# Optimization experiments

Measured on AMD Instinct MI355X. Metric: run time of the kernel, lower is better.

## Reference

```python
import jax, jax.numpy as jnp
import numpy as np

B, S, T, D, H, FF = 4, 96, 96, 512, 8, 2048
DK = D // H
EPS = 1e-5
NEG_SLOPE = 0.01  # LeakyReLU default


def setup_inputs() -> dict:
    key = jax.random.key(0)
    ks = jax.random.split(key, 8)
    w = lambda k, shape: jax.random.normal(k, shape, jnp.float32) * 0.02
    return {
        "x": jax.random.normal(ks[0], (B, S, T, D), jnp.float32),
        "mask_bias": jax.random.uniform(ks[1], (B, S, T), jnp.float32),
        "t_w": w(ks[2], (4, D, D)), "t_b": jnp.zeros((4, D), jnp.float32),
        "s_w": w(ks[3], (4, D, D)), "s_b": jnp.zeros((4, D), jnp.float32),
        "fc_w1": w(ks[4], (D, FF)), "fc_b1": jnp.zeros((FF,), jnp.float32),
        "fc_w2": w(ks[5], (FF, D)), "fc_b2": jnp.zeros((D,), jnp.float32),
        "ln1_g": jnp.ones((D,), jnp.float32), "ln1_b": jnp.zeros((D,), jnp.float32),
        "ln2_g": jnp.ones((D,), jnp.float32), "ln2_b": jnp.zeros((D,), jnp.float32),
    }


def _ln(y, g, b):
    m = y.mean(-1, keepdims=True)
    v = ((y - m) ** 2).mean(-1, keepdims=True)
    return (y - m) / jnp.sqrt(v + EPS) * g + b


def _split_heads(y):
    # (B,S,T,D) -> (B,H,S,T,DK)
    b, s, t, _ = y.shape
    return y.reshape(b, s, t, H, DK).transpose(0, 3, 1, 2, 4)


def _mha(x, w, b, mask_bias, time_axis):
    q = _split_heads(x @ w[0] + b[0])
    k = _split_heads(x @ w[1] + b[1])
    v = _split_heads(x @ w[2] + b[2])
    scale = 1.0 / np.sqrt(DK)
    if time_axis:
        # attention over time axis T: scores (B,H,S,T,T)
        p = jax.nn.softmax(jnp.einsum('bhstd,bhsud->bhstu', q, k) * scale, axis=-1)
        p = p * mask_bias[:, None, :, :, None]            # post-softmax mask
        o = jnp.einsum('bhstu,bhsud->bhstd', p, v)
    else:
        # attention over space axis S: scores (B,H,T,S,S)
        p = jax.nn.softmax(jnp.einsum('bhstd,bhutd->bhtsu', q, k) * scale, axis=-1)
        p = p * mask_bias.transpose(0, 2, 1)[:, None, :, :, None]
        o = jnp.einsum('bhtsu,bhutd->bhstd', p, v)
    o = o.transpose(0, 2, 3, 1, 4).reshape(x.shape)
    return o @ w[3] + b[3]


def reference(x, mask_bias, t_w, t_b, s_w, s_b, fc_w1, fc_b1, fc_w2, fc_b2,
              ln1_g, ln1_b, ln2_g, ln2_b):
    tt = _mha(x, t_w, t_b, mask_bias, True)
    ss = _mha(tt, s_w, s_b, mask_bias, False)
    x1 = _ln(x + ss, ln1_g, ln1_b)
    h = x1 @ fc_w1 + fc_b1
    h = jnp.where(h >= 0, h, NEG_SLOPE * h)
    ff = h @ fc_w2 + fc_b2
    return _ln(x1 + ff, ln2_g, ln2_b)
```

## Files before the change

### kernel.cpp

```cpp
#include <hip/hip_runtime.h>
#include <hip/hip_bf16.h>

#define B_ 4
#define S_ 96
#define T_ 96
#define D_ 512
#define H_ 8
#define FF_ 2048
#define NROWS (B_*S_*T_)
#define EPS_ 1e-5f
#define NEG_ 0.01f
#define DD_ (512*512)

typedef unsigned short u16;
typedef __attribute__((ext_vector_type(8))) short bf16x8;
typedef __attribute__((ext_vector_type(4))) float f32x4;
typedef __attribute__((address_space(1))) const unsigned glb_u32;
typedef __attribute__((address_space(3))) unsigned lds_u32;

__device__ __forceinline__ float bf(u16 u) { return __uint_as_float(((unsigned)u) << 16); }
__device__ __forceinline__ u16 f2bf(float f) {
    __hip_bfloat16 h = __float2bfloat16(f);
    return *reinterpret_cast<u16*>(&h);
}
__device__ __forceinline__ float blo(unsigned v) { return __uint_as_float(v << 16); }
__device__ __forceinline__ float bhi(unsigned v) { return __uint_as_float(v & 0xffff0000u); }

__device__ __forceinline__ float cvt_ld(float x) { return x; }
__device__ __forceinline__ float cvt_ld(u16 x)  { return bf(x); }
__device__ __forceinline__ void cvt_st(float* p, float v) { *p = v; }
__device__ __forceinline__ void cvt_st(u16* p, float v)   { *p = f2bf(v); }

__device__ __forceinline__ void load8(const float* p, float* y) {
    float4 a = *(const float4*)p, b = *(const float4*)(p + 4);
    y[0]=a.x; y[1]=a.y; y[2]=a.z; y[3]=a.w; y[4]=b.x; y[5]=b.y; y[6]=b.z; y[7]=b.w;
}
__device__ __forceinline__ void load8(const u16* p, float* y) {
    uint4 u = *(const uint4*)p;
    y[0]=blo(u.x); y[1]=bhi(u.x); y[2]=blo(u.y); y[3]=bhi(u.y);
    y[4]=blo(u.z); y[5]=bhi(u.z); y[6]=blo(u.w); y[7]=bhi(u.w);
}
__device__ __forceinline__ void store8(float* p, const float* y) {
    *(float4*)p       = make_float4(y[0], y[1], y[2], y[3]);
    *(float4*)(p + 4) = make_float4(y[4], y[5], y[6], y[7]);
}
__device__ __forceinline__ void store8(u16* p, const float* y) {
    ushort4 a, b;
    a.x = f2bf(y[0]); a.y = f2bf(y[1]); a.z = f2bf(y[2]); a.w = f2bf(y[3]);
    b.x = f2bf(y[4]); b.y = f2bf(y[5]); b.z = f2bf(y[6]); b.w = f2bf(y[7]);
    *(ushort4*)p = a; *(ushort4*)(p + 4) = b;
}

__global__ __launch_bounds__(256)
void cvt_f32_bf16(const float* __restrict__ in, u16* __restrict__ out)
{
    const size_t i = ((size_t)blockIdx.x * 256 + threadIdx.x) * 8;
    float y[8];
    load8(in + i, y);
    store8(out + i, y);
}

__global__ __launch_bounds__(256)
void tconv(const float* __restrict__ in, u16* __restrict__ out, int R, int C)
{
    __shared__ float t[32][33];
    const int c0 = blockIdx.x * 32, r0 = blockIdx.y * 32;
    const int tr = threadIdx.x >> 3, c4 = (threadIdx.x & 7) * 4;
    float4 v = *(const float4*)(in + (size_t)(r0 + tr) * C + c0 + c4);
    t[tr][c4] = v.x; t[tr][c4 + 1] = v.y; t[tr][c4 + 2] = v.z; t[tr][c4 + 3] = v.w;
    __syncthreads();
    const int oc = tr, r4 = c4;
    ushort4 u;
    u.x = f2bf(t[r4 + 0][oc]); u.y = f2bf(t[r4 + 1][oc]);
    u.z = f2bf(t[r4 + 2][oc]); u.w = f2bf(t[r4 + 3][oc]);
    *(ushort4*)(out + (size_t)(c0 + oc) * R + r0 + r4) = u;
}

__global__ __launch_bounds__(256)
void tconv8(const float* __restrict__ t_w, const float* __restrict__ s_w,
            u16* __restrict__ out)
{
    __shared__ float t[32][33];
    const int z = blockIdx.z;
    const float* in = (z < 4) ? (t_w + (size_t)z * DD_) : (s_w + (size_t)(z - 4) * DD_);
    u16* o = out + (size_t)z * DD_;
    const int c0 = blockIdx.x * 32, r0 = blockIdx.y * 32;
    const int tr = threadIdx.x >> 3, c4 = (threadIdx.x & 7) * 4;
    float4 v = *(const float4*)(in + (size_t)(r0 + tr) * 512 + c0 + c4);
    if (z == 3) {
        ushort4 u;
        u.x = f2bf(v.x); u.y = f2bf(v.y); u.z = f2bf(v.z); u.w = f2bf(v.w);
        *(ushort4*)(o + (size_t)(r0 + tr) * 512 + c0 + c4) = u;
        return;
    }
    t[tr][c4] = v.x; t[tr][c4 + 1] = v.y; t[tr][c4 + 2] = v.z; t[tr][c4 + 3] = v.w;
    __syncthreads();
    const int oc = tr, r4 = c4;
    ushort4 u;
    u.x = f2bf(t[r4 + 0][oc]); u.y = f2bf(t[r4 + 1][oc]);
    u.z = f2bf(t[r4 + 2][oc]); u.w = f2bf(t[r4 + 3][oc]);
    *(ushort4*)(o + (size_t)(c0 + oc) * 512 + r0 + r4) = u;
}

__global__ __launch_bounds__(256)
void fbias_k(const u16* __restrict__ WTs, const float* __restrict__ tb3,
             const float* __restrict__ sb, float* __restrict__ fb)
{
    const int j = blockIdx.x * 256 + threadIdx.x;
    const u16* row = WTs + (size_t)j * 512;
    float acc = sb[j];
    for (int k = 0; k < 512; k += 8) {
        float y[8], t[8];
        load8(row + k, y);
        load8(tb3 + k, t);
        acc += y[0]*t[0] + y[1]*t[1] + y[2]*t[2] + y[3]*t[3]
             + y[4]*t[4] + y[5]*t[5] + y[6]*t[6] + y[7]*t[7];
    }
    fb[j] = acc;
}

#define GEMM_PRE()                                                              \
    const int tid = threadIdx.x;                                                \
    const int w = tid >> 6, l = tid & 63;                                       \
    const int wr = w >> 1, wc = w & 1;                                          \
    const unsigned gx = gridDim.x;                                              \
    const unsigned nwg = gx * gridDim.y;                                        \
    unsigned f = blockIdx.y * gx + blockIdx.x;                                  \
    f = (f & 7) * (nwg >> 3) + (f >> 3);                                        \
    const int lrow = l >> 3;                                                    \
    const int swz8 = (((l & 7) ^ lrow) << 3);                                   \
    const int fr16 = l & 15;                                                    \
    const int kq = l >> 4;

#define GEMM_COMPUTE()                                                          \
    _Pragma("unroll")                                                           \
    for (int kk = 0; kk < 2; ++kk) {                                            \
        const int sw = ((((kk << 2) | kq)) ^ (fr16 & 7)) << 3;                  \
        bf16x8 af[4], bfr[4];                                                   \
        _Pragma("unroll")                                                       \
        for (int i = 0; i < 4; ++i)                                             \
            af[i] = *(bf16x8*)&As[(wr * 64 + i * 16 + fr16) * 64 + sw];         \
        _Pragma("unroll")                                                       \
        for (int j = 0; j < 4; ++j)                                             \
            bfr[j] = *(bf16x8*)&Bs[(wc * 64 + j * 16 + fr16) * 64 + sw];        \
        _Pragma("unroll")                                                       \
        for (int i = 0; i < 4; ++i)                                             \
            _Pragma("unroll")                                                   \
            for (int j = 0; j < 4; ++j)                                         \
                acc[i][j] = __builtin_amdgcn_mfma_f32_16x16x32_bf16(af[i], bfr[j], acc[i][j], 0, 0, 0); \
    }

template<int ACT, bool ACC, typename TC>
__global__ __launch_bounds__(256)
void gemm2(const u16* __restrict__ A, const u16* __restrict__ WT,
           const float* __restrict__ bias, TC* __restrict__ C,
           int K, int lda, int ldwt, int ldc)
{
    __shared__ u16 As[128 * 64];
    __shared__ u16 Bs[128 * 64];
    GEMM_PRE();
    const int row0 = (int)(f / gx) * 128, col0 = (int)(f % gx) * 128;
    f32x4 acc[4][4] = {};

    for (int kt = 0; kt < K; kt += 64) {
#pragma unroll
        for (int j = 0; j < 4; ++j) {
            const int line = w * 32 + j * 8;
            const u16* asrc = A  + (size_t)(row0 + line + lrow) * lda  + kt + swz8;
            const u16* bsrc = WT + (size_t)(col0 + line + lrow) * ldwt + kt + swz8;
            __builtin_amdgcn_global_load_lds((glb_u32*)asrc, (lds_u32*)&As[line * 64], 16, 0, 0);
            __builtin_amdgcn_global_load_lds((glb_u32*)bsrc, (lds_u32*)&Bs[line * 64], 16, 0, 0);
        }
        __syncthreads();
        GEMM_COMPUTE();
        __syncthreads();
    }
    const int crow = kq * 4;
#pragma unroll
    for (int i = 0; i < 4; ++i)
#pragma unroll
        for (int j = 0; j < 4; ++j) {
            const int col = col0 + wc * 64 + j * 16 + fr16;
            const float bv = (ACC || ACT == 2) ? 0.f : bias[col];
#pragma unroll
            for (int e = 0; e < 4; ++e) {
                const size_t r = (size_t)(row0 + wr * 64 + i * 16 + crow + e);
                TC* cp = &C[r * (size_t)ldc + col];
                float v = acc[i][j][e] + bv;
                if (ACC) v += cvt_ld(*cp);
                if (ACT == 1) v = (v >= 0.f) ? v : NEG_ * v;
                cvt_st(cp, v);
            }
        }
}

template<int ACT, typename TC>
__global__ __launch_bounds__(512)
void gemm3(const u16* __restrict__ A, const u16* __restrict__ WT,
           const float* __restrict__ bias,
           TC* __restrict__ p0, TC* __restrict__ p1, TC* __restrict__ p2,
           int K, int lda, int ldwt, int ldc, int pgshift)
{
    __shared__ u16 lds[65536];
    const int tid = threadIdx.x;
    const int w = tid >> 6, l = tid & 63;
    const int wr = w >> 2, wc = w & 3;
    const unsigned gx = gridDim.x;
    const unsigned nwg = gx * gridDim.y;
    unsigned f = blockIdx.y * gx + blockIdx.x;
    f = (f & 7) * (nwg >> 3) + (f >> 3);
    const int row0 = (int)(f / gx) * 256, colg0 = (int)(f % gx) * 256;
    const int lrow = l >> 3;
    const int swz8 = (((l & 7) ^ lrow) << 3);
    const int fr16 = l & 15;
    const int kq = l >> 4;

    f32x4 acc[8][4] = {};
    const int NT = K >> 6;

    auto stage = [&](int buf, int kt) {
        u16* Ad = lds + buf * 16384;
        u16* Bd = lds + 32768 + buf * 16384;
#pragma unroll
        for (int j = 0; j < 4; ++j) {
            const int lineb = j * 64 + w * 8;
            const int srow = lineb + lrow;
            const u16* asrc = A  + (size_t)(row0  + srow) * lda  + kt + swz8;
            const u16* bsrc = WT + (size_t)(colg0 + srow) * ldwt + kt + swz8;
            __builtin_amdgcn_global_load_lds((glb_u32*)asrc, (lds_u32*)&Ad[lineb * 64], 16, 0, 0);
            __builtin_amdgcn_global_load_lds((glb_u32*)bsrc, (lds_u32*)&Bd[lineb * 64], 16, 0, 0);
        }
    };

    stage(0, 0);
    for (int t = 0; t < NT; ++t) {
        const int cur = t & 1;
        if (t + 1 < NT) {
            stage(cur ^ 1, (t + 1) << 6);
            asm volatile("s_waitcnt vmcnt(8)" ::: "memory");
        } else {
            asm volatile("s_waitcnt vmcnt(0)" ::: "memory");
        }
        __builtin_amdgcn_s_barrier();
        const u16* Ab = lds + cur * 16384;
        const u16* Bb = lds + 32768 + cur * 16384;
        bf16x8 bq[4];
#pragma unroll
        for (int p = 0; p < 4; ++p) {
            const int kk = p >> 1, ih = p & 1;
            const int sw = ((((kk << 2) | kq)) ^ (fr16 & 7)) << 3;
            if (ih == 0) {
#pragma unroll
                for (int j = 0; j < 4; ++j)
                    bq[j] = *(bf16x8*)&Bb[(wc * 64 + j * 16 + fr16) * 64 + sw];
            }
            bf16x8 af[4];
#pragma unroll
            for (int i = 0; i < 4; ++i)
                af[i] = *(bf16x8*)&Ab[(wr * 128 + (ih * 4 + i) * 16 + fr16) * 64 + sw];
            __builtin_amdgcn_s_barrier();
            __builtin_amdgcn_s_setprio(1);
#pragma unroll
            for (int i = 0; i < 4; ++i)
#pragma unroll
                for (int j = 0; j < 4; ++j)
                    acc[ih * 4 + i][j] = __builtin_amdgcn_mfma_f32_16x16x32_bf16(
                        af[i], bq[j], acc[ih * 4 + i][j], 0, 0, 0);
            __builtin_amdgcn_s_setprio(0);
        }
    }
    const int crow = kq * 4;
#pragma unroll
    for (int i = 0; i < 8; ++i)
#pragma unroll
        for (int j = 0; j < 4; ++j) {
            const int colg = colg0 + wc * 64 + j * 16 + fr16;
            TC* Cb = (((unsigned)colg >> pgshift) == 0) ? p0
                   : (((unsigned)colg >> pgshift) == 1) ? p1 : p2;
            const int col = colg & ((1 << pgshift) - 1);
            const float bv = bias[colg];
#pragma unroll
            for (int e = 0; e < 4; ++e) {
                const size_t r = (size_t)(row0 + wr * 128 + i * 16 + crow + e);
                float v = acc[i][j][e] + bv;
                if (ACT == 1) v = (v >= 0.f) ? v : NEG_ * v;
                cvt_st(&Cb[r * (size_t)ldc + col], v);
            }
        }
}

__global__ __launch_bounds__(384)
void attn_mfma(const u16* __restrict__ q, const u16* __restrict__ kbuf,
               const u16* __restrict__ vbuf, const float* __restrict__ mask,
               u16* __restrict__ out, int time_axis)
{
    __shared__ __align__(16) u16 Ks[96][72];
    __shared__ __align__(16) u16 VT[64][104];
    __shared__ __align__(16) u16 Ps[96][104];
    const int g = blockIdx.x;
    const int h = g & 7;
    const int bs = g >> 3;
    const int b = bs / 96, st = bs % 96;
    const size_t base   = time_axis ? ((size_t)(b * 96 + st) * 96) : ((size_t)b * 9216 + st);
    const size_t stride = time_axis ? 1 : 96;
    const int tid = threadIdx.x;
    const int w = tid / 64, l = tid & 63;
    const int fr = l & 15, fk = (l >> 4) * 8;

    for (int task = tid; task < 96 * 8; task += 384) {
        const int r = task >> 3, c = task & 7;
        *(uint4*)&Ks[r][c * 8] =
            *(const uint4*)(kbuf + (base + (size_t)r * stride) * 512 + h * 64 + c * 8);
    }
    for (int task = tid; task < 96 * 8; task += 384) {
        const int r = task >> 3, c = task & 7;
        uint4 dv = *(const uint4*)(vbuf + (base + (size_t)r * stride) * 512 + h * 64 + c * 8);
        const u16* e = (const u16*)&dv;
#pragma unroll
        for (int j = 0; j < 8; ++j) VT[c * 8 + j][r] = e[j];
    }
    const u16* qp = q + (base + (size_t)(16 * w + fr) * stride) * 512 + h * 64;
    bf16x8 aq0 = *(const bf16x8*)(qp + fk);
    bf16x8 aq1 = *(const bf16x8*)(qp + 32 + fk);
    __syncthreads();

    f32x4 s[6] = {};
#pragma unroll
    for (int fc = 0; fc < 6; ++fc) {
        bf16x8 b0 = *(const bf16x8*)&Ks[fc * 16 + fr][fk];
        bf16x8 b1 = *(const bf16x8*)&Ks[fc * 16 + fr][32 + fk];
        s[fc] = __builtin_amdgcn_mfma_f32_16x16x32_bf16(aq0, b0, s[fc], 0, 0, 0);
        s[fc] = __builtin_amdgcn_mfma_f32_16x16x32_bf16(aq1, b1, s[fc], 0, 0, 0);
    }
    float mrow[4], lrow[4];
#pragma unroll
    for (int e = 0; e < 4; ++e) {
        float mx = s[0][e];
#pragma unroll
        for (int fc = 1; fc < 6; ++fc) mx = fmaxf(mx, s[fc][e]);
#pragma unroll
        for (int off = 1; off < 16; off <<= 1) mx = fmaxf(mx, __shfl_xor(mx, off));
        mrow[e] = mx * 0.125f;
        lrow[e] = 0.f;
    }
    const int e0 = (l >> 4) * 4;
#pragma unroll
    for (int fc = 0; fc < 6; ++fc) {
#pragma unroll
        for (int e = 0; e < 4; ++e) {
            const float p = __expf(fmaf(s[fc][e], 0.125f, -mrow[e]));
            lrow[e] += p;
            Ps[16 * w + e0 + e][fc * 16 + fr] = f2bf(p);
        }
    }
#pragma unroll
    for (int e = 0; e < 4; ++e)
#pragma unroll
        for (int off = 1; off < 16; off <<= 1) lrow[e] += __shfl_xor(lrow[e], off);

    __syncthreads();

    f32x4 oacc[4] = {};
#pragma unroll
    for (int ks = 0; ks < 3; ++ks) {
        bf16x8 ap = *(const bf16x8*)&Ps[16 * w + fr][ks * 32 + fk];
#pragma unroll
        for (int j = 0; j < 4; ++j) {
            bf16x8 bv = *(const bf16x8*)&VT[j * 16 + fr][ks * 32 + fk];
            oacc[j] = __builtin_amdgcn_mfma_f32_16x16x32_bf16(ap, bv, oacc[j], 0, 0, 0);
        }
    }
    float mk[4];
#pragma unroll
    for (int e = 0; e < 4; ++e) {
        const size_t qrow = base + (size_t)(16 * w + e0 + e) * stride;
        mk[e] = mask[qrow] / lrow[e];
    }
#pragma unroll
    for (int j = 0; j < 4; ++j)
#pragma unroll
        for (int e = 0; e < 4; ++e) {
            const size_t qrow = base + (size_t)(16 * w + e0 + e) * stride;
            out[qrow * 512 + h * 64 + j * 16 + fr] = f2bf(oacc[j][e] * mk[e]);
        }
}

template<typename TA, typename TB, typename TO>
__global__ __launch_bounds__(64)
void add_ln(const TA* __restrict__ a, const TB* __restrict__ bsrc,
            const float* __restrict__ g, const float* __restrict__ beta,
            TO* __restrict__ out)
{
    const size_t row = blockIdx.x;
    const int lane = threadIdx.x;
    float ya[8], yb[8], y[8];
    load8(a + row * D_ + lane * 8, ya);
    load8(bsrc + row * D_ + lane * 8, yb);
    float sum = 0.f, sq = 0.f;
#pragma unroll
    for (int i = 0; i < 8; ++i) { y[i] = ya[i] + yb[i]; sum += y[i]; sq += y[i] * y[i]; }
#pragma unroll
    for (int off = 32; off >= 1; off >>= 1) {
        sum += __shfl_xor(sum, off);
        sq  += __shfl_xor(sq, off);
    }
    const float mean = sum * (1.f / D_);
    const float var  = sq * (1.f / D_) - mean * mean;
    const float rstd = rsqrtf(var + EPS_);
    const float* gp = g + lane * 8;
    const float* bp = beta + lane * 8;
    float o[8];
#pragma unroll
    for (int i = 0; i < 8; ++i) o[i] = (y[i] - mean) * rstd * gp[i] + bp[i];
    store8(out + row * D_ + lane * 8, o);
}

extern "C" void kernel_launch(void* const* d_in, const int* in_sizes, int n_in,
                              void* d_out, int out_size, void* d_ws, size_t ws_size,
                              hipStream_t stream)
{
    const float* x     = (const float*)d_in[0];
    const float* mask  = (const float*)d_in[1];
    const float* t_w   = (const float*)d_in[2];
    const float* t_b   = (const float*)d_in[3];
    const float* s_w   = (const float*)d_in[4];
    const float* s_b   = (const float*)d_in[5];
    const float* fc_w1 = (const float*)d_in[6];
    const float* fc_b1 = (const float*)d_in[7];
    const float* fc_w2 = (const float*)d_in[8];
    const float* fc_b2 = (const float*)d_in[9];
    const float* ln1_g = (const float*)d_in[10];
    const float* ln1_b = (const float*)d_in[11];
    const float* ln2_g = (const float*)d_in[12];
    const float* ln2_b = (const float*)d_in[13];

    const size_t PG = (size_t)NROWS * 512;
    const size_t WTC = (size_t)2048 * 512 * 2;
    if (ws_size < (PG * 3 + WTC) * sizeof(u16)) return;
    u16* O0   = (u16*)d_out;
    u16* O1   = O0 + PG;
    u16* WS0  = (u16*)d_ws;
    u16* WS1  = WS0 + PG;
    u16* WS2  = WS1 + PG;
    u16* TAIL = WS0 + 3 * PG;

    const dim3 gblk(256);
    const dim3 g512(4, NROWS / 128);
    const dim3 qkv3grid(6, NROWS / 256);
    const dim3 h3grid(8, 72);

    cvt_f32_bf16<<<dim3((unsigned)(PG / 2048)), gblk, 0, stream>>>(x, WS2);
    tconv8<<<dim3(16, 16, 8), gblk, 0, stream>>>(t_w, s_w, TAIL);
    gemm3<0, u16><<<qkv3grid, dim3(512), 0, stream>>>(
        WS2, TAIL, t_b, O0, WS0, WS1, 512, 512, 512, 512, 9);
    gemm2<2, false, u16><<<dim3(4, 12), gblk, 0, stream>>>(
        TAIL + (size_t)4 * DD_, TAIL + (size_t)3 * DD_, nullptr, TAIL, 512, 512, 512, 512);
    float* fb = (float*)(TAIL + (size_t)3 * DD_);
    fbias_k<<<dim3(6), gblk, 0, stream>>>(TAIL + (size_t)4 * DD_, t_b + 3 * 512, s_b, fb);
    attn_mfma<<<dim3(B_ * H_ * 96), dim3(384), 0, stream>>>(O0, WS0, WS1, mask, O0, 1);
    gemm3<0, u16><<<qkv3grid, dim3(512), 0, stream>>>(
        O0, TAIL, fb, O1, WS0, WS1, 512, 512, 512, 512, 9);
    attn_mfma<<<dim3(B_ * H_ * 96), dim3(384), 0, stream>>>(O1, WS0, WS1, mask, O0, 0);
    gemm2<0, false, u16><<<g512, gblk, 0, stream>>>(
        O0, TAIL + (size_t)7 * DD_, s_b + 3 * 512, O1, 512, 512, 512, 512);
    add_ln<u16, u16, u16><<<dim3(NROWS), dim3(64), 0, stream>>>(WS2, O1, ln1_g, ln1_b, WS2);
    u16* WT1f = TAIL;
    u16* WT2f = TAIL + (size_t)2048 * 512;
    tconv<<<dim3(64, 16), gblk, 0, stream>>>(fc_w1, WT1f, 512, 2048);
    tconv<<<dim3(16, 64), gblk, 0, stream>>>(fc_w2, WT2f, 2048, 512);
    for (int r = 0; r < 2; ++r) {
        const size_t off = (size_t)r * 18432;
        gemm3<1, u16><<<h3grid, dim3(512), 0, stream>>>(
            WS2 + off * 512, WT1f, fc_b1, O0, O0, O0, 512, 512, 512, 2048, 30);
        gemm2<0, false, u16><<<dim3(4, 144), gblk, 0, stream>>>(
            O0, WT2f, fc_b2, WS1 + off * 512, 2048, 2048, 2048, 512);
    }
    add_ln<u16, u16, float><<<dim3(NROWS), dim3(64), 0, stream>>>(
        WS2, WS1, ln2_g, ln2_b, (float*)d_out);
}
```

Measured before the change: 553.4 us.

## Halve gemm3 K-tile to 32 with new swizzle and use gemm3 for output projection

The 256x256 gemm3 kernel now stages K in chunks of 32 instead of 64. This halves LDS use to 64KB, which may allow more workgroups per CU, and replaces the per-substep barrier with a single barrier at the end of each tile. The LDS swizzle is redesigned for the 32-wide rows. The spatial output projection moves from the smaller-tile gemm2 to gemm3 with a 2x144 grid. In exchange the kernel runs twice as many K iterations and barriers, and the output projection launches fewer, larger workgroups.

```diff
diff --git a/kernel.cpp b/kernel.cpp
--- a/kernel.cpp
+++ b/kernel.cpp
@@ -201,7 +201,7 @@
            TC* __restrict__ p0, TC* __restrict__ p1, TC* __restrict__ p2,
            int K, int lda, int ldwt, int ldc, int pgshift)
 {
-    __shared__ u16 lds[65536];
+    __shared__ u16 lds[32768];
     const int tid = threadIdx.x;
     const int w = tid >> 6, l = tid & 63;
     const int wr = w >> 2, wc = w & 3;
@@ -210,25 +210,25 @@
     unsigned f = blockIdx.y * gx + blockIdx.x;
     f = (f & 7) * (nwg >> 3) + (f >> 3);
     const int row0 = (int)(f / gx) * 256, colg0 = (int)(f % gx) * 256;
-    const int lrow = l >> 3;
-    const int swz8 = (((l & 7) ^ lrow) << 3);
     const int fr16 = l & 15;
     const int kq = l >> 4;
+    const int kc = ((kq ^ ((fr16 >> 1) & 3)) << 3);
 
     f32x4 acc[8][4] = {};
-    const int NT = K >> 6;
+    const int NT = K >> 5;
 
     auto stage = [&](int buf, int kt) {
-        u16* Ad = lds + buf * 16384;
-        u16* Bd = lds + 32768 + buf * 16384;
-#pragma unroll
-        for (int j = 0; j < 4; ++j) {
-            const int lineb = j * 64 + w * 8;
-            const int srow = lineb + lrow;
-            const u16* asrc = A  + (size_t)(row0  + srow) * lda  + kt + swz8;
-            const u16* bsrc = WT + (size_t)(colg0 + srow) * ldwt + kt + swz8;
-            __builtin_amdgcn_global_load_lds((glb_u32*)asrc, (lds_u32*)&Ad[lineb * 64], 16, 0, 0);
-            __builtin_amdgcn_global_load_lds((glb_u32*)bsrc, (lds_u32*)&Bd[lineb * 64], 16, 0, 0);
+        u16* Ad = lds + buf * 8192;
+        u16* Bd = lds + 16384 + buf * 8192;
+        const int sk = (((l & 3) ^ ((l >> 3) & 3)) << 3);
+#pragma unroll
+        for (int part = 0; part < 2; ++part) {
+            const int lineb = part * 128 + w * 16;
+            const int line  = lineb + (l >> 2);
+            const u16* asrc = A  + (size_t)(row0  + line) * lda  + kt + sk;
+            const u16* bsrc = WT + (size_t)(colg0 + line) * ldwt + kt + sk;
+            __builtin_amdgcn_global_load_lds((glb_u32*)asrc, (lds_u32*)&Ad[lineb * 32], 16, 0, 0);
+            __builtin_amdgcn_global_load_lds((glb_u32*)bsrc, (lds_u32*)&Bd[lineb * 32], 16, 0, 0);
         }
     };
 
@@ -236,29 +236,24 @@
     for (int t = 0; t < NT; ++t) {
         const int cur = t & 1;
         if (t + 1 < NT) {
-            stage(cur ^ 1, (t + 1) << 6);
-            asm volatile("s_waitcnt vmcnt(8)" ::: "memory");
+            stage(cur ^ 1, (t + 1) << 5);
+            asm volatile("s_waitcnt vmcnt(4)" ::: "memory");
         } else {
             asm volatile("s_waitcnt vmcnt(0)" ::: "memory");
         }
         __builtin_amdgcn_s_barrier();
-        const u16* Ab = lds + cur * 16384;
-        const u16* Bb = lds + 32768 + cur * 16384;
+        const u16* Ab = lds + cur * 8192;
+        const u16* Bb = lds + 16384 + cur * 8192;
         bf16x8 bq[4];
 #pragma unroll
-        for (int p = 0; p < 4; ++p) {
-            const int kk = p >> 1, ih = p & 1;
-            const int sw = ((((kk << 2) | kq)) ^ (fr16 & 7)) << 3;
-            if (ih == 0) {
-#pragma unroll
-                for (int j = 0; j < 4; ++j)
-                    bq[j] = *(bf16x8*)&Bb[(wc * 64 + j * 16 + fr16) * 64 + sw];
-            }
+        for (int j = 0; j < 4; ++j)
+            bq[j] = *(bf16x8*)&Bb[(wc * 64 + j * 16 + fr16) * 32 + kc];
+#pragma unroll
+        for (int ih = 0; ih < 2; ++ih) {
             bf16x8 af[4];
 #pragma unroll
             for (int i = 0; i < 4; ++i)
-                af[i] = *(bf16x8*)&Ab[(wr * 128 + (ih * 4 + i) * 16 + fr16) * 64 + sw];
-            __builtin_amdgcn_s_barrier();
+                af[i] = *(bf16x8*)&Ab[(wr * 128 + (ih * 4 + i) * 16 + fr16) * 32 + kc];
             __builtin_amdgcn_s_setprio(1);
 #pragma unroll
             for (int i = 0; i < 4; ++i)
@@ -268,6 +263,9 @@
                         af[i], bq[j], acc[ih * 4 + i][j], 0, 0, 0);
             __builtin_amdgcn_s_setprio(0);
         }
+        asm volatile("s_waitcnt lgkmcnt(0)" ::: "memory");
+        __builtin_amdgcn_sched_barrier(0);
+        __builtin_amdgcn_s_barrier();
     }
     const int crow = kq * 4;
 #pragma unroll
@@ -445,8 +443,8 @@
     u16* TAIL = WS0 + 3 * PG;
 
     const dim3 gblk(256);
-    const dim3 g512(4, NROWS / 128);
     const dim3 qkv3grid(6, NROWS / 256);
+    const dim3 ss3grid(2, NROWS / 256);
     const dim3 h3grid(8, 72);
 
     cvt_f32_bf16<<<dim3((unsigned)(PG / 2048)), gblk, 0, stream>>>(x, WS2);
@@ -461,8 +459,8 @@
     gemm3<0, u16><<<qkv3grid, dim3(512), 0, stream>>>(
         O0, TAIL, fb, O1, WS0, WS1, 512, 512, 512, 512, 9);
     attn_mfma<<<dim3(B_ * H_ * 96), dim3(384), 0, stream>>>(O1, WS0, WS1, mask, O0, 0);
-    gemm2<0, false, u16><<<g512, gblk, 0, stream>>>(
-        O0, TAIL + (size_t)7 * DD_, s_b + 3 * 512, O1, 512, 512, 512, 512);
+    gemm3<0, u16><<<ss3grid, dim3(512), 0, stream>>>(
+        O0, TAIL + (size_t)7 * DD_, s_b + 3 * 512, O1, O1, O1, 512, 512, 512, 512, 30);
     add_ln<u16, u16, u16><<<dim3(NROWS), dim3(64), 0, stream>>>(WS2, O1, ln1_g, ln1_b, WS2);
     u16* WT1f = TAIL;
     u16* WT2f = TAIL + (size_t)2048 * 512;
```

After: 578.3 us. +4.5%, slower.
